# Kernel optimization log

Hardware: AMD Instinct MI355X
Metric: run time of the kernel (lower is better)

## Reference

```python
import jax, jax.numpy as jnp
import numpy as np


def setup_inputs() -> dict:
    key = jax.random.key(0)
    k1, k2, k3, k4 = jax.random.split(key, 4)
    B, C, H, W = 8, 64, 64, 64
    Cr = C // 8
    x = jax.random.normal(k1, (B, C, H, W), dtype=jnp.float32)
    Wf = jax.random.normal(k2, (Cr, C), dtype=jnp.float32) * (1.0 / np.sqrt(C))
    Wg = jax.random.normal(k3, (Cr, C), dtype=jnp.float32) * (1.0 / np.sqrt(C))
    Wh = jax.random.normal(k4, (C, C), dtype=jnp.float32) * (1.0 / np.sqrt(C))
    gamma = jnp.zeros((1,), dtype=jnp.float32)
    return {"x": x, "Wf": Wf, "Wg": Wg, "Wh": Wh, "gamma": gamma}


def reference(x, Wf, Wg, Wh, gamma):
    B, C, H, W = x.shape
    N = H * W
    xf = x.reshape(B, C, N)                      # [B, C, N]
    fx = jnp.einsum("oc,bcn->bno", Wf, xf)       # queries [B, N, C/8]
    gx = jnp.einsum("oc,bcn->bon", Wg, xf)       # keys    [B, C/8, N]
    hx = jnp.einsum("oc,bcn->bon", Wh, xf)       # values  [B, C,   N]
    beta = jnp.einsum("bnd,bdm->bnm", fx, gx)    # [B, N, N], no 1/sqrt(d) scale (SAGAN)
    beta = jax.nn.softmax(beta, axis=-1)
    # o = bmm(hx, beta^T): o[b,c,i] = sum_j hx[b,c,j] * beta[b,i,j]
    o = jnp.einsum("bcj,bij->bci", hx, beta)     # [B, C, N]
    o = o.reshape(B, C, H, W)
    return gamma * o + x
```

## Files before the change

### kernel.cpp

```cpp
#include <hip/hip_runtime.h>
#include <hip/hip_bf16.h>


#define N_ 4096
#define LOG2E 1.4426950408889634f

typedef __attribute__((ext_vector_type(8)))  __bf16 bf16x8;
typedef __attribute__((ext_vector_type(2)))  float  f32x2;
typedef __attribute__((ext_vector_type(4)))  float  f32x4;
typedef __attribute__((ext_vector_type(16))) float  f32x16;

union U16B { uint4 u; bf16x8 b; };

static __device__ inline uint pack_bf2(float a, float b) {
  __hip_bfloat162 h = __float22bfloat162_rn(make_float2(a, b));
  uint r; __builtin_memcpy(&r, &h, 4); return r;
}
static __device__ inline ushort f2bf(float a) {
  __hip_bfloat16 h = __float2bfloat16(a);
  ushort r; __builtin_memcpy(&r, &h, 2); return r;
}
static __device__ inline float bflo(uint u) {
  uint v = u << 16; float f; __builtin_memcpy(&f, &v, 4); return f;
}
static __device__ inline float bfhi(uint u) {
  uint v = u & 0xffff0000u; float f; __builtin_memcpy(&f, &v, 4); return f;
}
static __device__ inline uint fexp2i(float s) {
  return (uint)(int)(s * 8388608.0f + 1065353216.0f);
}
static __device__ inline float asf(uint u) {
  float f; __builtin_memcpy(&f, &u, 4); return f;
}

__global__ __launch_bounds__(256) void prep_kernel(
    const float* __restrict__ x,  const float* __restrict__ Wf,
    const float* __restrict__ Wg, const float* __restrict__ Wh,
    ushort* __restrict__ Qp, ushort* __restrict__ Kp, ushort* __restrict__ Vf)
{
  __shared__ __align__(16) char smem[37376];
  float*  T   = (float*)smem;
  ushort* xTl = (ushort*)(smem + 16640);
  ushort* Wb  = (ushort*)(smem + 25856);
  const int bid = blockIdx.x;
  const int b = bid & 7, tile = bid >> 3, n0 = tile * 64;
  const int tid = threadIdx.x;

  {
    const int nl = tid & 63, cw = tid >> 6;
#pragma unroll
    for (int i = 0; i < 16; ++i) {
      const int c = i * 4 + cw;
      T[c * 65 + nl] = x[((size_t)(b * 64 + c)) * N_ + n0 + nl];
    }
  }
  {
#pragma unroll
    for (int i = 0; i < 20; ++i) {
      const int e = i * 256 + tid;
      const int row = e >> 6, col = e & 63;
      float v;
      if (row < 8)       v = Wf[row * 64 + col] * LOG2E;
      else if (row < 16) v = Wg[(row - 8) * 64 + col];
      else               v = Wh[(row - 16) * 64 + col];
      Wb[row * 72 + col] = f2bf(v);
    }
  }
  __syncthreads();
  {
    const int n = tid >> 2, cq = (tid & 3) * 16;
    uint o[8];
#pragma unroll
    for (int j = 0; j < 8; ++j)
      o[j] = pack_bf2(T[(cq + 2 * j) * 65 + n], T[(cq + 2 * j + 1) * 65 + n]);
    *(uint4*)(xTl + n * 72 + cq)     = make_uint4(o[0], o[1], o[2], o[3]);
    *(uint4*)(xTl + n * 72 + cq + 8) = make_uint4(o[4], o[5], o[6], o[7]);
  }
  __syncthreads();

  const int l = tid & 63, w = tid >> 6, l15 = l & 15, lq = l >> 4;
  const int nn = w * 16 + l15;
  U16B bf0, bf1;
  bf0.u = *(const uint4*)(xTl + nn * 72 + lq * 8);
  bf1.u = *(const uint4*)(xTl + nn * 72 + 32 + lq * 8);
  f32x4 acc[5];
#pragma unroll
  for (int mt = 0; mt < 5; ++mt) {
    U16B a0, a1;
    a0.u = *(const uint4*)(Wb + (mt * 16 + l15) * 72 + lq * 8);
    a1.u = *(const uint4*)(Wb + (mt * 16 + l15) * 72 + 32 + lq * 8);
    f32x4 c0 = __builtin_amdgcn_mfma_f32_16x16x32_bf16(a0.b, bf0.b, (f32x4){0.f,0.f,0.f,0.f}, 0, 0, 0);
    acc[mt]  = __builtin_amdgcn_mfma_f32_16x16x32_bf16(a1.b, bf1.b, c0, 0, 0, 0);
  }
  const int n = n0 + nn;
  {
    uint lo = pack_bf2(acc[0][0], acc[0][1]);
    uint hi = pack_bf2(acc[0][2], acc[0][3]);
    ushort* dst = (lq < 2 ? Qp : Kp) + ((size_t)(b * N_ + n)) * 8 + (lq & 1) * 4;
    *(uint2*)dst = make_uint2(lo, hi);
  }
  ushort* Vt = (ushort*)smem;
  const int jp = nn;
  const int jl = jp & 31, stp = (jl >> 4) & 1, j16 = jl & 15;
  const int s  = (j16 & 3) | ((j16 & 4) << 1) | ((j16 & 8) >> 1);
  const int vbase = ((jp >> 5) * 2 + stp) * 1024 + (s >> 3) * 256 + (s & 7);
#pragma unroll
  for (int mt = 1; mt < 5; ++mt)
#pragma unroll
    for (int r = 0; r < 4; ++r) {
      const int c = (mt - 1) * 16 + lq * 4 + r;
      Vt[vbase + (c >> 5) * 512 + (c & 31) * 8] = f2bf(acc[mt][r]);
    }
  __syncthreads();
  const uint4* src = (const uint4*)Vt;
  uint4* dst = (uint4*)(Vf + ((size_t)(b * 64 + tile)) * 4096);
  dst[tid]       = src[tid];
  dst[256 + tid] = src[256 + tid];
}

__global__ __launch_bounds__(512, 4) void attn_kernel(
    const ushort* __restrict__ Qp, const ushort* __restrict__ Kp,
    const ushort* __restrict__ Vf,
    ushort* __restrict__ Opart, float* __restrict__ Lpart)
{
  __shared__ __align__(16) uint4 smem4[2048];
  uint4* vsl = smem4;
  uint4* Kl  = smem4 + 1024;
  const int bid = blockIdx.x;
  const int b = bid & 7, js = (bid >> 3) & 3, qblk = bid >> 5;
  const int tid = threadIdx.x, w = tid >> 6, l = tid & 63;
  const int l31 = l & 31, lq1 = l >> 5;
  const int q0w = qblk * 256 + w * 32;
  const int jb0 = js * 1024;
  const uint4 zero4 = make_uint4(0u, 0u, 0u, 0u);

  const uint4* Kg = (const uint4*)(Kp + ((size_t)(b * N_ + jb0)) * 8);
  Kl[tid]       = Kg[tid];
  Kl[512 + tid] = Kg[512 + tid];
  const uint4* Vg = (const uint4*)(Vf + ((size_t)(b * 64 + js * 16)) * 4096);
  vsl[tid] = Vg[tid];

  U16B qf;
  qf.u = lq1 ? zero4 : *(const uint4*)(Qp + ((size_t)(b * N_ + q0w + l31)) * 8);

  const f32x16 Oz = {0,0,0,0,0,0,0,0,0,0,0,0,0,0,0,0};
  f32x16 O[2] = {Oz, Oz};
  f32x2 Lv = {0.f, 0.f};
  uint4 vp;
  int p = 0;
  __syncthreads();

  for (int jt = 0; jt < 16; ++jt) {
    if (jt < 15) vp = Vg[(jt + 1) * 512 + tid];
    const uint4* vb = vsl + p * 512;
#pragma unroll
    for (int jc = 0; jc < 2; ++jc) {
      U16B kf; kf.u = Kl[jt * 64 + jc * 32 + l31];
      f32x16 St = __builtin_amdgcn_mfma_f32_32x32x16_bf16(kf.b, qf.b, Oz, 0, 0, 0);
      uint ib[16];
#pragma unroll
      for (int r = 0; r < 16; ++r) ib[r] = fexp2i(St[r]);
      f32x2 t0 = {asf(ib[0]), asf(ib[1])},  t1 = {asf(ib[2]),  asf(ib[3])};
      f32x2 t2 = {asf(ib[4]), asf(ib[5])},  t3 = {asf(ib[6]),  asf(ib[7])};
      f32x2 t4 = {asf(ib[8]), asf(ib[9])},  t5 = {asf(ib[10]), asf(ib[11])};
      f32x2 t6 = {asf(ib[12]), asf(ib[13])}, t7 = {asf(ib[14]), asf(ib[15])};
      Lv += ((t0 + t1) + (t2 + t3)) + ((t4 + t5) + (t6 + t7));
      uint pk[8];
#pragma unroll
      for (int d = 0; d < 8; ++d)
        pk[d] = __builtin_amdgcn_perm(ib[2 * d + 1], ib[2 * d], 0x07060302u);
#pragma unroll
      for (int h = 0; h < 2; ++h) {
        U16B pa;
        pa.u = make_uint4(pk[h * 4], pk[h * 4 + 1], pk[h * 4 + 2], pk[h * 4 + 3]);
        const int ks = jc * 2 + h;
#pragma unroll
        for (int ch = 0; ch < 2; ++ch) {
          U16B vfr; vfr.u = vb[ks * 128 + ch * 64 + l];
          O[ch] = __builtin_amdgcn_mfma_f32_32x32x16_bf16(pa.b, vfr.b, O[ch], 0, 0, 0);
        }
      }
    }
    if (jt < 15) vsl[(p ^ 1) * 512 + tid] = vp;
    __syncthreads();
    p ^= 1;
  }

  float L = Lv.x + Lv.y;
  L += __shfl_xor(L, 32);
  if (lq1 == 0)
    Lpart[((size_t)(js * 8 + b)) * N_ + q0w + l31] = L;

  ushort* Op = Opart + (((size_t)(js * 8 + b)) * N_ + q0w) * 64;
#pragma unroll
  for (int ch = 0; ch < 2; ++ch)
#pragma unroll
    for (int g = 0; g < 4; ++g)
#pragma unroll
      for (int r = 0; r < 4; ++r) {
        const int q = r + 8 * g + 4 * lq1;
        Op[q * 64 + ch * 32 + l31] = f2bf(O[ch][g * 4 + r]);
      }
}

__global__ __launch_bounds__(256) void combine_kernel(
    const ushort* __restrict__ Opart, const float* __restrict__ Lpart,
    const float* __restrict__ x, const float* __restrict__ gamma,
    float* __restrict__ out)
{
  __shared__ float T[64 * 65];
  const int bid = blockIdx.x;
  const int b = bid & 7, n0 = (bid >> 3) * 64;
  const int tid = threadIdx.x;
  float acc[16];
#pragma unroll
  for (int e = 0; e < 16; ++e) acc[e] = 0.f;
#pragma unroll
  for (int js = 0; js < 4; ++js) {
    const ushort* Op = Opart + (((size_t)(js * 8 + b)) * N_ + n0) * 64 + tid * 16;
    uint4 a  = *(const uint4*)Op;
    uint4 c2 = *(const uint4*)(Op + 8);
    acc[0] += bflo(a.x);  acc[1] += bfhi(a.x);  acc[2] += bflo(a.y);  acc[3] += bfhi(a.y);
    acc[4] += bflo(a.z);  acc[5] += bfhi(a.z);  acc[6] += bflo(a.w);  acc[7] += bfhi(a.w);
    acc[8] += bflo(c2.x); acc[9] += bfhi(c2.x); acc[10]+= bflo(c2.y); acc[11]+= bfhi(c2.y);
    acc[12]+= bflo(c2.z); acc[13]+= bfhi(c2.z); acc[14]+= bflo(c2.w); acc[15]+= bfhi(c2.w);
  }
  const int nr = tid >> 2, c0 = (tid & 3) * 16;
#pragma unroll
  for (int e = 0; e < 16; ++e) T[nr * 65 + c0 + e] = acc[e];
  __syncthreads();
  const float g = gamma[0];
  const int n = tid & 63, cq = (tid >> 6) * 16;
  float Ls = 0.f;
#pragma unroll
  for (int js = 0; js < 4; ++js) Ls += Lpart[((size_t)(js * 8 + b)) * N_ + n0 + n];
  const float gr = g / Ls;
#pragma unroll
  for (int i = 0; i < 16; ++i) {
    const int c = cq + i;
    const size_t oi = ((size_t)(b * 64 + c)) * N_ + n0 + n;
    out[oi] = gr * T[n * 65 + c] + x[oi];
  }
}

extern "C" void kernel_launch(void* const* d_in, const int* in_sizes, int n_in,
                              void* d_out, int out_size, void* d_ws, size_t ws_size,
                              hipStream_t stream) {
  const float* x     = (const float*)d_in[0];
  const float* Wf    = (const float*)d_in[1];
  const float* Wg    = (const float*)d_in[2];
  const float* Wh    = (const float*)d_in[3];
  const float* gamma = (const float*)d_in[4];
  float* out = (float*)d_out;
  char* ws = (char*)d_ws;

  ushort* Qp    = (ushort*)(ws);
  ushort* Kp    = (ushort*)(ws + 512 * 1024);
  ushort* Vf    = (ushort*)(ws + 1024 * 1024);
  float*  Lpart = (float*) (ws + 5 * 1024 * 1024);
  ushort* Opart = (ushort*)(ws + 6 * 1024 * 1024);

  prep_kernel   <<<512, 256, 0, stream>>>(x, Wf, Wg, Wh, Qp, Kp, Vf);
  attn_kernel   <<<512, 512, 0, stream>>>(Qp, Kp, Vf, Opart, Lpart);
  combine_kernel<<<512, 256, 0, stream>>>(Opart, Lpart, x, gamma, out);
}
```

Measured before the change: 106.7 us.

## Software-pipeline score computation one tile ahead and deepen V prefetch

Restructures the attention loop so the QK^T MFMA, exp2 approximation and bf16 packing for tile jt+1 are computed right after the PV MFMAs of tile jt. The aim is to overlap exp/VALU work with matrix-core work. V global loads are now prefetched two tiles ahead using two rotating registers. __syncthreads is replaced by an inline-asm lgkmcnt wait plus s_barrier, which avoids waiting on outstanding global loads. In exchange, register pressure rises because packed P values and an extra V prefetch register stay live, and the hand-written barrier relies on LDS ordering being correct.

```diff
diff --git a/kernel.cpp b/kernel.cpp
--- a/kernel.cpp
+++ b/kernel.cpp
@@ -31,6 +31,9 @@
 }
 static __device__ inline float asf(uint u) {
   float f; __builtin_memcpy(&f, &u, 4); return f;
+}
+static __device__ inline void lds_barrier() {
+  asm volatile("s_waitcnt lgkmcnt(0)\n\ts_barrier" ::: "memory");
 }
 
 __global__ __launch_bounds__(256) void prep_kernel(
@@ -139,6 +142,7 @@
   Kl[512 + tid] = Kg[512 + tid];
   const uint4* Vg = (const uint4*)(Vf + ((size_t)(b * 64 + js * 16)) * 4096);
   vsl[tid] = Vg[tid];
+  uint4 vp1 = Vg[512 + tid];
 
   U16B qf;
   qf.u = lq1 ? zero4 : *(const uint4*)(Qp + ((size_t)(b * N_ + q0w + l31)) * 8);
@@ -146,33 +150,38 @@
   const f32x16 Oz = {0,0,0,0,0,0,0,0,0,0,0,0,0,0,0,0};
   f32x16 O[2] = {Oz, Oz};
   f32x2 Lv = {0.f, 0.f};
-  uint4 vp;
+  uint pk[2][8];
+  lds_barrier();
+
+#pragma unroll
+  for (int jc = 0; jc < 2; ++jc) {
+    U16B kf; kf.u = Kl[jc * 32 + l31];
+    f32x16 St = __builtin_amdgcn_mfma_f32_32x32x16_bf16(kf.b, qf.b, Oz, 0, 0, 0);
+    uint ib[16];
+#pragma unroll
+    for (int r = 0; r < 16; ++r) ib[r] = fexp2i(St[r]);
+    f32x2 t0 = {asf(ib[0]), asf(ib[1])},  t1 = {asf(ib[2]),  asf(ib[3])};
+    f32x2 t2 = {asf(ib[4]), asf(ib[5])},  t3 = {asf(ib[6]),  asf(ib[7])};
+    f32x2 t4 = {asf(ib[8]), asf(ib[9])},  t5 = {asf(ib[10]), asf(ib[11])};
+    f32x2 t6 = {asf(ib[12]), asf(ib[13])}, t7 = {asf(ib[14]), asf(ib[15])};
+    Lv += ((t0 + t1) + (t2 + t3)) + ((t4 + t5) + (t6 + t7));
+#pragma unroll
+    for (int d = 0; d < 8; ++d)
+      pk[jc][d] = __builtin_amdgcn_perm(ib[2 * d + 1], ib[2 * d], 0x07060302u);
+  }
+
   int p = 0;
-  __syncthreads();
-
   for (int jt = 0; jt < 16; ++jt) {
-    if (jt < 15) vp = Vg[(jt + 1) * 512 + tid];
+    uint4 vp2 = zero4;
+    if (jt < 14) vp2 = Vg[(jt + 2) * 512 + tid];
     const uint4* vb = vsl + p * 512;
 #pragma unroll
-    for (int jc = 0; jc < 2; ++jc) {
-      U16B kf; kf.u = Kl[jt * 64 + jc * 32 + l31];
-      f32x16 St = __builtin_amdgcn_mfma_f32_32x32x16_bf16(kf.b, qf.b, Oz, 0, 0, 0);
-      uint ib[16];
-#pragma unroll
-      for (int r = 0; r < 16; ++r) ib[r] = fexp2i(St[r]);
-      f32x2 t0 = {asf(ib[0]), asf(ib[1])},  t1 = {asf(ib[2]),  asf(ib[3])};
-      f32x2 t2 = {asf(ib[4]), asf(ib[5])},  t3 = {asf(ib[6]),  asf(ib[7])};
-      f32x2 t4 = {asf(ib[8]), asf(ib[9])},  t5 = {asf(ib[10]), asf(ib[11])};
-      f32x2 t6 = {asf(ib[12]), asf(ib[13])}, t7 = {asf(ib[14]), asf(ib[15])};
-      Lv += ((t0 + t1) + (t2 + t3)) + ((t4 + t5) + (t6 + t7));
-      uint pk[8];
-#pragma unroll
-      for (int d = 0; d < 8; ++d)
-        pk[d] = __builtin_amdgcn_perm(ib[2 * d + 1], ib[2 * d], 0x07060302u);
+    for (int jc = 0; jc < 2; ++jc)
 #pragma unroll
       for (int h = 0; h < 2; ++h) {
         U16B pa;
-        pa.u = make_uint4(pk[h * 4], pk[h * 4 + 1], pk[h * 4 + 2], pk[h * 4 + 3]);
+        pa.u = make_uint4(pk[jc][h * 4], pk[jc][h * 4 + 1],
+                          pk[jc][h * 4 + 2], pk[jc][h * 4 + 3]);
         const int ks = jc * 2 + h;
 #pragma unroll
         for (int ch = 0; ch < 2; ++ch) {
@@ -180,10 +189,28 @@
           O[ch] = __builtin_amdgcn_mfma_f32_32x32x16_bf16(pa.b, vfr.b, O[ch], 0, 0, 0);
         }
       }
-    }
-    if (jt < 15) vsl[(p ^ 1) * 512 + tid] = vp;
-    __syncthreads();
+    if (jt < 15) {
+#pragma unroll
+      for (int jc = 0; jc < 2; ++jc) {
+        U16B kf; kf.u = Kl[(jt + 1) * 64 + jc * 32 + l31];
+        f32x16 St = __builtin_amdgcn_mfma_f32_32x32x16_bf16(kf.b, qf.b, Oz, 0, 0, 0);
+        uint ib[16];
+#pragma unroll
+        for (int r = 0; r < 16; ++r) ib[r] = fexp2i(St[r]);
+        f32x2 t0 = {asf(ib[0]), asf(ib[1])},  t1 = {asf(ib[2]),  asf(ib[3])};
+        f32x2 t2 = {asf(ib[4]), asf(ib[5])},  t3 = {asf(ib[6]),  asf(ib[7])};
+        f32x2 t4 = {asf(ib[8]), asf(ib[9])},  t5 = {asf(ib[10]), asf(ib[11])};
+        f32x2 t6 = {asf(ib[12]), asf(ib[13])}, t7 = {asf(ib[14]), asf(ib[15])};
+        Lv += ((t0 + t1) + (t2 + t3)) + ((t4 + t5) + (t6 + t7));
+#pragma unroll
+        for (int d = 0; d < 8; ++d)
+          pk[jc][d] = __builtin_amdgcn_perm(ib[2 * d + 1], ib[2 * d], 0x07060302u);
+      }
+      vsl[(p ^ 1) * 512 + tid] = vp1;
+    }
+    lds_barrier();
     p ^= 1;
+    vp1 = vp2;
   }
 
   float L = Lv.x + Lv.y;
```

Result: no change. 105.8 us (-0.9%).
